# Performance work log

Hardware: AMD Instinct MI355X
Metric: run time of the kernel (lower is better)

The kernel has to match this reference:

```python
import jax, jax.numpy as jnp
import numpy as np

EMB_DIM = 128
HEAD_SIZE = 16  # embDim // numHea = 128 // 8


def setup_inputs() -> dict:
    key = jax.random.key(0)
    k1, k2, k3, k4 = jax.random.split(key, 4)
    B, T = 8, 2048
    inpEmb = jax.random.normal(k1, (B, T, EMB_DIM), dtype=jnp.float32)
    # nn.Linear(embDim, heaSiz, bias=False) weights, stored transposed so y = x @ W
    Wq = jax.random.normal(k2, (EMB_DIM, HEAD_SIZE), dtype=jnp.float32) / np.sqrt(EMB_DIM)
    Wk = jax.random.normal(k3, (EMB_DIM, HEAD_SIZE), dtype=jnp.float32) / np.sqrt(EMB_DIM)
    Wv = jax.random.normal(k4, (EMB_DIM, HEAD_SIZE), dtype=jnp.float32) / np.sqrt(EMB_DIM)
    return {"inpEmb": inpEmb, "Wq": Wq, "Wk": Wk, "Wv": Wv}


def reference(inpEmb, Wq, Wk, Wv):
    # q,k,v: [B, T, H]
    q = inpEmb @ Wq
    k = inpEmb @ Wk
    v = inpEmb @ Wv
    scale = HEAD_SIZE ** -0.5
    # scores: [B, T, T]
    scores = jnp.einsum('bqh,bkh->bqk', q, k) * scale
    T = inpEmb.shape[1]
    causal = jnp.tril(jnp.ones((T, T), dtype=bool))
    scores = jnp.where(causal, scores, -jnp.inf)
    weights = jax.nn.softmax(scores, axis=-1)
    # dropout treated as identity (eval mode) for deterministic reference
    return jnp.einsum('bqk,bkh->bqh', weights, v)
```

## Files before the change

### kernel.cpp

```cpp
#include <hip/hip_runtime.h>
#include <hip/hip_bf16.h>

#define T_SEQ 2048
#define EMB   128
#define H     16
#define BATCH 8
#define VSTR  2064
#define QSCALE 0.360673760222241f

#define EXP2F(x) __builtin_amdgcn_exp2f(x)

typedef short short8_t __attribute__((ext_vector_type(8)));
typedef float f32x4    __attribute__((ext_vector_type(4)));

__device__ __forceinline__ unsigned short f2bf(float f) {
    __hip_bfloat16 h = __float2bfloat16(f);
    return *reinterpret_cast<unsigned short*>(&h);
}

__global__ __launch_bounds__(192) void qkv_kernel(
    const float* __restrict__ x,
    const float* __restrict__ Wq,
    const float* __restrict__ Wk,
    const float* __restrict__ Wv,
    unsigned short* __restrict__ Qbf,
    unsigned short* __restrict__ Kbf,
    unsigned short* __restrict__ Vt)
{
    const int tid  = threadIdx.x;
    const int wv   = tid >> 6;
    const int lane = tid & 63;
    const int q    = lane >> 4;
    const int n    = lane & 15;
    const int r0   = blockIdx.x * 16;

    const float* Wm = (wv == 0) ? Wq : (wv == 1) ? Wk : Wv;
    const float* xr = x + (size_t)(r0 + n) * EMB;

    f32x4 a = {0.f, 0.f, 0.f, 0.f};
#pragma unroll
    for (int t = 0; t < 4; ++t) {
        const int k0 = t * 32 + q * 8;
        float4 xa = *reinterpret_cast<const float4*>(xr + k0);
        float4 xb = *reinterpret_cast<const float4*>(xr + k0 + 4);
        union { unsigned short s[8]; short8_t v; } xf;
        xf.s[0]=f2bf(xa.x); xf.s[1]=f2bf(xa.y); xf.s[2]=f2bf(xa.z); xf.s[3]=f2bf(xa.w);
        xf.s[4]=f2bf(xb.x); xf.s[5]=f2bf(xb.y); xf.s[6]=f2bf(xb.z); xf.s[7]=f2bf(xb.w);
        union { unsigned short s[8]; short8_t v; } wf;
#pragma unroll
        for (int j = 0; j < 8; ++j)
            wf.s[j] = f2bf(Wm[(size_t)(k0 + j) * H + n]);
        a = __builtin_amdgcn_mfma_f32_16x16x32_bf16(xf.v, wf.v, a, 0, 0, 0);
    }

    const int grow = r0 + q * 4;
    if (wv == 0) {
#pragma unroll
        for (int r = 0; r < 4; ++r)
            Qbf[(size_t)(grow + r) * H + n] = f2bf(a[r] * QSCALE);
    } else if (wv == 1) {
#pragma unroll
        for (int r = 0; r < 4; ++r)
            Kbf[(size_t)(grow + r) * H + n] = f2bf(a[r]);
    } else {
        const int b   = grow >> 11;
        const int ib0 = grow & 2047;
        union { unsigned short s[4]; unsigned long long u; } vp;
        vp.s[0]=f2bf(a[0]); vp.s[1]=f2bf(a[1]); vp.s[2]=f2bf(a[2]); vp.s[3]=f2bf(a[3]);
        *reinterpret_cast<unsigned long long*>(
            Vt + ((size_t)b * H + n) * VSTR + ib0) = vp.u;
    }
}

__global__ __launch_bounds__(256, 4) void attn_fused(
    const unsigned short* __restrict__ Qbf,
    const unsigned short* __restrict__ Kbf,
    const unsigned short* __restrict__ Vt,
    float* __restrict__ out)
{
    __shared__ unsigned int Pbuf[4][16][68];
    __shared__ float CombA[4][16][20];
    __shared__ float CombL[4][16];

    const int qt = (T_SEQ / 16 - 1) - blockIdx.x;
    const int b  = blockIdx.y;
    const int i0 = qt << 4;
    const int nc = (qt >> 3) + 1;

    const int tid  = threadIdx.x;
    const int wv   = tid >> 6;
    const int lane = tid & 63;
    const int q    = lane >> 4;
    const int n    = lane & 15;
    const int irow = i0 + n;

    const unsigned short* Qp = Qbf + (size_t)b * T_SEQ * H;
    const unsigned short* Kp = Kbf + (size_t)b * T_SEQ * H;
    const unsigned short* vrow = Vt + (size_t)b * H * VSTR + (size_t)n * VSTR;

    short8_t qf = {0,0,0,0,0,0,0,0};
    if (q < 2)
        qf = *reinterpret_cast<const short8_t*>(Qp + (size_t)irow * H + q * 8);

    f32x4 acc = {0.f, 0.f, 0.f, 0.f};
    float l = 0.f;

    int c = wv;
    short8_t kcur[8];
#pragma unroll
    for (int s = 0; s < 8; ++s) kcur[s] = (short8_t){0,0,0,0,0,0,0,0};
    if (c < nc && q < 2) {
        const int j0 = c << 7;
#pragma unroll
        for (int s = 0; s < 8; ++s)
            kcur[s] = *reinterpret_cast<const short8_t*>(
                          Kp + (size_t)(j0 + s * 16 + n) * H + q * 8);
    }

    for (; c < nc; c += 4) {
        const int j0 = c << 7;

        f32x4 S[8];
#pragma unroll
        for (int s = 0; s < 8; ++s) {
            f32x4 z = {0.f, 0.f, 0.f, 0.f};
            S[s] = __builtin_amdgcn_mfma_f32_16x16x32_bf16(kcur[s], qf, z, 0, 0, 0);
        }
        const int c2 = c + 4;
        if (c2 < nc && q < 2) {
            const int j2 = c2 << 7;
#pragma unroll
            for (int s = 0; s < 8; ++s)
                kcur[s] = *reinterpret_cast<const short8_t*>(
                              Kp + (size_t)(j2 + s * 16 + n) * H + q * 8);
        }
        short8_t vf[4];
#pragma unroll
        for (int h = 0; h < 4; ++h)
            vf[h] = *reinterpret_cast<const short8_t*>(vrow + j0 + h * 32 + q * 8);

        if (j0 + 127 > i0) {
#pragma unroll
            for (int s = 0; s < 8; ++s) {
                const int kb = j0 + s * 16 + q * 4;
#pragma unroll
                for (int rr = 0; rr < 4; ++rr)
                    S[s][rr] = (kb + rr <= irow) ? S[s][rr] : -1e30f;
            }
        }

        float lc = 0.f;
#pragma unroll
        for (int s = 0; s < 8; ++s) {
            float e0 = EXP2F(S[s][0]);
            float e1 = EXP2F(S[s][1]);
            float e2 = EXP2F(S[s][2]);
            float e3 = EXP2F(S[s][3]);
            lc += (e0 + e1) + (e2 + e3);
            unsigned int b0 = __builtin_bit_cast(unsigned int, e0);
            unsigned int b1 = __builtin_bit_cast(unsigned int, e1);
            unsigned int b2 = __builtin_bit_cast(unsigned int, e2);
            unsigned int b3 = __builtin_bit_cast(unsigned int, e3);
            unsigned long long pw =
                (unsigned long long)((b1 & 0xffff0000u) | (b0 >> 16)) |
                ((unsigned long long)((b3 & 0xffff0000u) | (b2 >> 16)) << 32);
            *reinterpret_cast<unsigned long long*>(&Pbuf[wv][n][8 * s + 2 * q]) = pw;
        }
        l += lc;

#pragma unroll
        for (int h = 0; h < 4; ++h) {
            uint4 p4 = *reinterpret_cast<const uint4*>(&Pbuf[wv][n][16 * h + 4 * q]);
            union { uint4 u; short8_t v; } pu; pu.u = p4;
            acc = __builtin_amdgcn_mfma_f32_16x16x32_bf16(vf[h], pu.v, acc, 0, 0, 0);
        }
    }

    l += __shfl_xor(l, 16);
    l += __shfl_xor(l, 32);

    *reinterpret_cast<float4*>(&CombA[wv][n][4 * q]) =
        (float4){acc[0], acc[1], acc[2], acc[3]};
    if (q == 0) CombL[wv][n] = l;
    __syncthreads();

    {
        const int row = tid >> 4;
        const int d   = tid & 15;
        float L = 0.f, O = 0.f;
#pragma unroll
        for (int w = 0; w < 4; ++w) {
            L += CombL[w][row];
            O += CombA[w][row][d];
        }
        out[((size_t)b * T_SEQ + i0 + row) * H + d] = O / L;
    }
}

extern "C" void kernel_launch(void* const* d_in, const int* in_sizes, int n_in,
                              void* d_out, int out_size, void* d_ws, size_t ws_size,
                              hipStream_t stream)
{
    const float* x  = (const float*)d_in[0];
    const float* Wq = (const float*)d_in[1];
    const float* Wk = (const float*)d_in[2];
    const float* Wv = (const float*)d_in[3];
    float* out = (float*)d_out;

    const size_t NE = (size_t)BATCH * T_SEQ * H;
    unsigned short* Qbf = (unsigned short*)d_ws;
    unsigned short* Kbf = Qbf + NE;
    unsigned short* Vt  = Kbf + NE;

    qkv_kernel<<<BATCH * T_SEQ / 16, 192, 0, stream>>>(
        x, Wq, Wk, Wv, Qbf, Kbf, Vt);
    attn_fused<<<dim3(T_SEQ / 16, BATCH), 256, 0, stream>>>(Qbf, Kbf, Vt, out);
}
```

Measured before the change: 75.91 us.

## Fuse Q projection into attention kernel, projecting only K and V beforehand

The Q projection moves out of the separate projection kernel and into the attention kernel. Each wave computes the 16x16 Q tile from x and Wq with MFMA and passes it through a small shared buffer to form its Q fragment. This removes the global write and read of the Q tensor and shrinks the projection kernel to two waves per block. In exchange, all four waves of every attention block redundantly recompute the same Q tile, and that projection now sits on the attention kernel's critical path.

New measurement: 80.60 us. 1.06x slower.

```diff
diff --git a/kernel.cpp b/kernel.cpp
--- a/kernel.cpp
+++ b/kernel.cpp
@@ -18,12 +18,10 @@
     return *reinterpret_cast<unsigned short*>(&h);
 }
 
-__global__ __launch_bounds__(192) void qkv_kernel(
+__global__ __launch_bounds__(128) void kv_kernel(
     const float* __restrict__ x,
-    const float* __restrict__ Wq,
     const float* __restrict__ Wk,
     const float* __restrict__ Wv,
-    unsigned short* __restrict__ Qbf,
     unsigned short* __restrict__ Kbf,
     unsigned short* __restrict__ Vt)
 {
@@ -34,7 +32,7 @@
     const int n    = lane & 15;
     const int r0   = blockIdx.x * 16;
 
-    const float* Wm = (wv == 0) ? Wq : (wv == 1) ? Wk : Wv;
+    const float* Wm = (wv == 0) ? Wk : Wv;
     const float* xr = x + (size_t)(r0 + n) * EMB;
 
     f32x4 a = {0.f, 0.f, 0.f, 0.f};
@@ -55,10 +53,6 @@
 
     const int grow = r0 + q * 4;
     if (wv == 0) {
-#pragma unroll
-        for (int r = 0; r < 4; ++r)
-            Qbf[(size_t)(grow + r) * H + n] = f2bf(a[r] * QSCALE);
-    } else if (wv == 1) {
 #pragma unroll
         for (int r = 0; r < 4; ++r)
             Kbf[(size_t)(grow + r) * H + n] = f2bf(a[r]);
@@ -73,7 +67,8 @@
 }
 
 __global__ __launch_bounds__(256, 4) void attn_fused(
-    const unsigned short* __restrict__ Qbf,
+    const float* __restrict__ x,
+    const float* __restrict__ Wq,
     const unsigned short* __restrict__ Kbf,
     const unsigned short* __restrict__ Vt,
     float* __restrict__ out)
@@ -81,6 +76,7 @@
     __shared__ unsigned int Pbuf[4][16][68];
     __shared__ float CombA[4][16][20];
     __shared__ float CombL[4][16];
+    __shared__ unsigned short Qtmp[4][16][16];
 
     const int qt = (T_SEQ / 16 - 1) - blockIdx.x;
     const int b  = blockIdx.y;
@@ -94,16 +90,8 @@
     const int n    = lane & 15;
     const int irow = i0 + n;
 
-    const unsigned short* Qp = Qbf + (size_t)b * T_SEQ * H;
     const unsigned short* Kp = Kbf + (size_t)b * T_SEQ * H;
     const unsigned short* vrow = Vt + (size_t)b * H * VSTR + (size_t)n * VSTR;
-
-    short8_t qf = {0,0,0,0,0,0,0,0};
-    if (q < 2)
-        qf = *reinterpret_cast<const short8_t*>(Qp + (size_t)irow * H + q * 8);
-
-    f32x4 acc = {0.f, 0.f, 0.f, 0.f};
-    float l = 0.f;
 
     int c = wv;
     short8_t kcur[8];
@@ -116,6 +104,34 @@
             kcur[s] = *reinterpret_cast<const short8_t*>(
                           Kp + (size_t)(j0 + s * 16 + n) * H + q * 8);
     }
+
+    {
+        const float* xr = x + ((size_t)b * T_SEQ + i0 + n) * EMB;
+        f32x4 aq = {0.f, 0.f, 0.f, 0.f};
+#pragma unroll
+        for (int t = 0; t < 4; ++t) {
+            const int k0 = t * 32 + q * 8;
+            float4 xa = *reinterpret_cast<const float4*>(xr + k0);
+            float4 xb = *reinterpret_cast<const float4*>(xr + k0 + 4);
+            union { unsigned short s[8]; short8_t v; } xf;
+            xf.s[0]=f2bf(xa.x); xf.s[1]=f2bf(xa.y); xf.s[2]=f2bf(xa.z); xf.s[3]=f2bf(xa.w);
+            xf.s[4]=f2bf(xb.x); xf.s[5]=f2bf(xb.y); xf.s[6]=f2bf(xb.z); xf.s[7]=f2bf(xb.w);
+            union { unsigned short s[8]; short8_t v; } wf;
+#pragma unroll
+            for (int j = 0; j < 8; ++j)
+                wf.s[j] = f2bf(Wq[(size_t)(k0 + j) * H + n]);
+            aq = __builtin_amdgcn_mfma_f32_16x16x32_bf16(xf.v, wf.v, aq, 0, 0, 0);
+        }
+#pragma unroll
+        for (int r = 0; r < 4; ++r)
+            Qtmp[wv][4 * q + r][n] = f2bf(aq[r] * QSCALE);
+    }
+    short8_t qf = {0,0,0,0,0,0,0,0};
+    if (q < 2)
+        qf = *reinterpret_cast<const short8_t*>(&Qtmp[wv][n][8 * q]);
+
+    f32x4 acc = {0.f, 0.f, 0.f, 0.f};
+    float l = 0.f;
 
     for (; c < nc; c += 4) {
         const int j0 = c << 7;
@@ -208,11 +224,10 @@
     float* out = (float*)d_out;
 
     const size_t NE = (size_t)BATCH * T_SEQ * H;
-    unsigned short* Qbf = (unsigned short*)d_ws;
-    unsigned short* Kbf = Qbf + NE;
+    unsigned short* Kbf = (unsigned short*)d_ws;
     unsigned short* Vt  = Kbf + NE;
 
-    qkv_kernel<<<BATCH * T_SEQ / 16, 192, 0, stream>>>(
-        x, Wq, Wk, Wv, Qbf, Kbf, Vt);
-    attn_fused<<<dim3(T_SEQ / 16, BATCH), 256, 0, stream>>>(Qbf, Kbf, Vt, out);
-}
+    kv_kernel<<<BATCH * T_SEQ / 16, 128, 0, stream>>>(x, Wk, Wv, Kbf, Vt);
+    attn_fused<<<dim3(T_SEQ / 16, BATCH), 256, 0, stream>>>(
+        x, Wq, Kbf, Vt, out);
+}
```
